# Kernel optimization log

Measured on AMD Instinct MI355X. Metric: run time of the kernel, lower is better.

Reference implementation:

```python
import jax, jax.numpy as jnp
import numpy as np

D_MODEL = 1024
N_HEADS = 16
HEAD_DIM = D_MODEL // N_HEADS
WINDOW = 512


def _rope(q, k, seq_len, head_dim):
    # interleaved RoPE, identical to the torch implementation
    theta = 1.0 / 10000.0 ** (jnp.arange(0, head_dim, 2, dtype=jnp.float32) / head_dim)
    pos = jnp.arange(seq_len, dtype=jnp.float32)
    freqs = jnp.outer(pos, theta)                      # [S, hD/2]
    cos_f = jnp.cos(freqs)[None, None]                 # [1,1,S,hD/2]
    sin_f = jnp.sin(freqs)[None, None]

    def rotate(x):
        x1, x2 = x[..., ::2], x[..., 1::2]
        return jnp.stack([x1 * cos_f - x2 * sin_f, x1 * sin_f + x2 * cos_f], axis=-1).reshape(x.shape)

    return rotate(q), rotate(k)


def _sliding_window_attn(q, k, v, W, scale):
    # chunked O(S*W) causal sliding-window attention
    B, nH, S, hD = q.shape
    n_chunks = (S + W - 1) // W
    pad_s = n_chunks * W - S
    k_pad = jnp.pad(k, ((0, 0), (0, 0), (W, pad_s), (0, 0)))
    v_pad = jnp.pad(v, ((0, 0), (0, 0), (W, pad_s), (0, 0)))
    q_pad = jnp.pad(q, ((0, 0), (0, 0), (0, pad_s), (0, 0)))
    q_c = q_pad.reshape(B, nH, n_chunks, W, hD)
    k_r = k_pad.reshape(B, nH, n_chunks + 1, W, hD)
    v_r = v_pad.reshape(B, nH, n_chunks + 1, W, hD)
    # window i = chunks [i, i+1] of the left-padded sequence (== torch unfold)
    k_c = jnp.concatenate([k_r[:, :, :-1], k_r[:, :, 1:]], axis=3)  # [B,nH,C,2W,hD]
    v_c = jnp.concatenate([v_r[:, :, :-1], v_r[:, :, 1:]], axis=3)
    attn = jnp.einsum('bhcqd,bhckd->bhcqk', q_c, k_c) * scale

    qi = jnp.arange(W)[:, None]
    ki = jnp.arange(2 * W)[None, :]
    cw_mask = (ki <= qi) | (ki > qi + W)               # [W, 2W]
    chunk_idx = jnp.arange(n_chunks)[:, None]
    abs_k = chunk_idx * W + ki - W                     # [C, 2W]
    pad_mask = (abs_k < 0) | (abs_k >= S)
    q_pos = jnp.arange(n_chunks * W).reshape(n_chunks, W)
    full_mask = cw_mask[None] | pad_mask[:, None, :] | (q_pos >= S)[..., None]  # [C,W,2W]

    attn = jnp.where(full_mask[None, None], -jnp.inf, attn)
    attn = jax.nn.softmax(attn, axis=-1)
    attn = jnp.nan_to_num(attn, nan=0.0)
    out = jnp.einsum('bhcqk,bhckd->bhcqd', attn, v_c)
    return out.reshape(B, nH, n_chunks * W, hD)[:, :, :S]


def _rmsnorm(x, w):
    eps = jnp.finfo(x.dtype).eps
    return x * jax.lax.rsqrt(jnp.mean(x * x, axis=-1, keepdims=True) + eps) * w


def _sdpa(q, k, v, scale):
    s = jnp.einsum('bhqd,bhkd->bhqk', q, k) * scale
    return jnp.einsum('bhqk,bhkd->bhqd', jax.nn.softmax(s, axis=-1), v)


def setup_inputs() -> dict:
    key = jax.random.key(0)
    ks = jax.random.split(key, 11)
    D = D_MODEL
    std = 0.02
    return {
        'x': jax.random.normal(ks[0], (2, 4096, D), jnp.float32),
        'landmarks': jax.random.normal(ks[1], (2, 256, D), jnp.float32),
        'archived_landmarks': jax.random.normal(ks[2], (2, 128, D), jnp.float32),
        'W_qkv': jax.random.normal(ks[3], (D, 3 * D), jnp.float32) * std,
        'W_lm': jax.random.normal(ks[4], (D, 2 * D), jnp.float32) * std,
        'W_arch': jax.random.normal(ks[5], (D, 2 * D), jnp.float32) * std,
        'W_o': jax.random.normal(ks[6], (D, D), jnp.float32) * std,
        'W_gate': jax.random.normal(ks[7], (3 * D, 2 * D), jnp.float32) * std,
        'g_local': jnp.ones((D,), jnp.float32),
        'g_lm': jnp.ones((D,), jnp.float32),
        'g_arch': jnp.ones((D,), jnp.float32),
    }


def reference(x, landmarks, archived_landmarks, W_qkv, W_lm, W_arch, W_o, W_gate, g_local, g_lm, g_arch):
    B, S, D = x.shape
    nH, hD = N_HEADS, HEAD_DIM
    scale = hD ** -0.5

    def rsh(t, L):
        return jnp.transpose(t.reshape(B, L, nH, hD), (0, 2, 1, 3))

    q, k, v = jnp.split(x @ W_qkv, 3, axis=-1)
    Q, K, V = rsh(q, S), rsh(k, S), rsh(v, S)
    Q, K = _rope(Q, K, S, hD)

    Weff = min(WINDOW, S)
    out_loc = _sliding_window_attn(Q, K, V, Weff, scale)  # S > Weff -> chunked path
    out_loc = _rmsnorm(jnp.transpose(out_loc, (0, 2, 1, 3)).reshape(B, S, D), g_local)

    L = landmarks.shape[1]
    K_lm, V_lm = jnp.split(landmarks @ W_lm, 2, axis=-1)
    out_lm = _sdpa(Q, rsh(K_lm, L), rsh(V_lm, L), scale)
    out_lm = _rmsnorm(jnp.transpose(out_lm, (0, 2, 1, 3)).reshape(B, S, D), g_lm)

    A = archived_landmarks.shape[1]
    K_a, V_a = jnp.split(archived_landmarks @ W_arch, 2, axis=-1)
    out_a = _sdpa(Q, rsh(K_a, A), rsh(V_a, A), scale)
    out_a = _rmsnorm(jnp.transpose(out_a, (0, 2, 1, 3)).reshape(B, S, D), g_arch)

    concat = jnp.concatenate([out_loc, out_lm, out_a], axis=-1)
    gate, value = jnp.split(concat @ W_gate, 2, axis=-1)
    return (jax.nn.silu(gate) * value) @ W_o
```

## Files before the change

### kernel.cpp

```cpp
#include <hip/hip_runtime.h>
#include <cstdint>
#include <cstddef>

typedef __bf16 bf16;
typedef __bf16 bf16x2 __attribute__((ext_vector_type(2)));
typedef __bf16 bf16x4 __attribute__((ext_vector_type(4)));
typedef __bf16 bf16x8 __attribute__((ext_vector_type(8)));
typedef float  f32x2 __attribute__((ext_vector_type(2)));
typedef float  f32x4 __attribute__((ext_vector_type(4)));

#define DEVFN __device__ __forceinline__
#define BAR()  asm volatile("s_barrier" ::: "memory")
#define VMW0() asm volatile("s_waitcnt vmcnt(0)" ::: "memory")
#define VMW3() asm volatile("s_waitcnt vmcnt(3)" ::: "memory")
#define VMW4() asm volatile("s_waitcnt vmcnt(4)" ::: "memory")

DEVFN void gld_lds16(void* lds, const void* g) {
  __builtin_amdgcn_global_load_lds(
      (__attribute__((address_space(1))) void*)g,
      (__attribute__((address_space(3))) void*)lds,
      16, 0, 0);
}

__global__ void cast_f32_bf16(const float* __restrict__ in, bf16* __restrict__ out, int n4) {
  int i = blockIdx.x * blockDim.x + threadIdx.x;
  if (i < n4) {
    f32x4 v = reinterpret_cast<const f32x4*>(in)[i];
    bf16x4 o;
    o[0] = (bf16)v[0]; o[1] = (bf16)v[1]; o[2] = (bf16)v[2]; o[3] = (bf16)v[3];
    reinterpret_cast<bf16x4*>(out)[i] = o;
  }
}

__global__ void transpose_cast(const float* __restrict__ in, bf16* __restrict__ out,
                               int R, int C) {
  __shared__ float t[32][33];
  int tx = threadIdx.x, ty = threadIdx.y;
  int c = blockIdx.x * 32 + tx;
  #pragma unroll
  for (int j = 0; j < 4; ++j) {
    int r = blockIdx.y * 32 + ty + j * 8;
    t[ty + j * 8][tx] = in[(size_t)r * C + c];
  }
  __syncthreads();
  int rr = blockIdx.y * 32 + tx;
  #pragma unroll
  for (int j = 0; j < 4; ++j) {
    int cc = blockIdx.x * 32 + ty + j * 8;
    out[(size_t)cc * R + rr] = (bf16)t[tx][ty + j * 8];
  }
}

__global__ void rope_table(float* __restrict__ tab) {
  int idx = blockIdx.x * 256 + threadIdx.x;
  int s = idx >> 5, i = idx & 31;
  float theta = powf(10000.f, -(float)(2 * i) * (1.f / 64.f));
  float f = (float)s * theta;
  tab[idx * 2]     = cosf(f);
  tab[idx * 2 + 1] = sinf(f);
}

template<typename OT>
__global__ __launch_bounds__(512) void gemm256(
    const bf16* __restrict__ A, const bf16* __restrict__ Bt, OT* __restrict__ C,
    int M, int N, int K) {
  __shared__ alignas(16) bf16 lds[2][2][2][256 * 32];
  const int tid = threadIdx.x;
  const int w = tid >> 6, l = tid & 63;
  const int l15 = l & 15, lg = l >> 4;
  const int wm = w >> 2, wn = w & 3;
  const int nwg = gridDim.x, qx = nwg >> 3;
  const int swz = (blockIdx.x & 7) * qx + (blockIdx.x >> 3);
  const int gx = N >> 8;
  const int m0 = (swz / gx) << 8;
  const int n0 = (swz % gx) << 8;
  const int nt = K >> 6;

  auto stage = [&](int b, int ab, int kk, int t) {
    const bf16* __restrict__ src = ab ? Bt : A;
    const int base0 = ab ? n0 : m0;
    const int k0 = (t << 6) + (kk << 5);
    #pragma unroll
    for (int i = 0; i < 2; ++i) {
      int u = i * 512 + tid;
      int row = u >> 2, slot = u & 3;
      int sslot = slot ^ ((row >> 1) & 3);
      gld_lds16(&lds[b][ab][kk][(i * 512 + w * 64) * 8],
                src + (size_t)(base0 + row) * K + k0 + sslot * 8);
    }
  };
  auto rd = [&](int b, int ab, int kk, int r) -> bf16x8 {
    return *reinterpret_cast<const bf16x8*>(
        &lds[b][ab][kk][(r << 5) + ((lg ^ ((r >> 1) & 3)) << 3)]);
  };

  f32x4 acc[8][4] = {};
  bf16x8 aLo[4], aHi[4], bfr[4];

  stage(0, 0, 0, 0);
  stage(0, 1, 0, 0);
  stage(0, 0, 1, 0);
  stage(0, 1, 1, 0);
  VMW4();
  BAR();

  for (int t = 0; t < nt; ++t) {
    const int c = t & 1;
    const bool st = (t + 1) < nt;
    #pragma unroll
    for (int f = 0; f < 4; ++f) aLo[f] = rd(c, 0, 0, wm * 128 + f * 16 + l15);
    #pragma unroll
    for (int f = 0; f < 4; ++f) bfr[f] = rd(c, 1, 0, wn * 64 + f * 16 + l15);
    if (st) stage(c ^ 1, 0, 0, t + 1);
    BAR();
    __builtin_amdgcn_s_setprio(1);
    #pragma unroll
    for (int mi = 0; mi < 4; ++mi)
      #pragma unroll
      for (int ni = 0; ni < 4; ++ni)
        acc[mi][ni] = __builtin_amdgcn_mfma_f32_16x16x32_bf16(aLo[mi], bfr[ni], acc[mi][ni], 0, 0, 0);
    __builtin_amdgcn_s_setprio(0);
    #pragma unroll
    for (int f = 0; f < 4; ++f) aHi[f] = rd(c, 0, 0, wm * 128 + (f + 4) * 16 + l15);
    BAR();
    if (st) stage(c ^ 1, 1, 0, t + 1);
    BAR();
    __builtin_amdgcn_s_setprio(1);
    #pragma unroll
    for (int mi = 0; mi < 4; ++mi)
      #pragma unroll
      for (int ni = 0; ni < 4; ++ni)
        acc[mi + 4][ni] = __builtin_amdgcn_mfma_f32_16x16x32_bf16(aHi[mi], bfr[ni], acc[mi + 4][ni], 0, 0, 0);
    __builtin_amdgcn_s_setprio(0);
    if (st) { VMW4(); } else { VMW0(); }
    BAR();
    #pragma unroll
    for (int f = 0; f < 4; ++f) aLo[f] = rd(c, 0, 1, wm * 128 + f * 16 + l15);
    #pragma unroll
    for (int f = 0; f < 4; ++f) bfr[f] = rd(c, 1, 1, wn * 64 + f * 16 + l15);
    if (st) stage(c ^ 1, 0, 1, t + 1);
    BAR();
    __builtin_amdgcn_s_setprio(1);
    #pragma unroll
    for (int mi = 0; mi < 4; ++mi)
      #pragma unroll
      for (int ni = 0; ni < 4; ++ni)
        acc[mi][ni] = __builtin_amdgcn_mfma_f32_16x16x32_bf16(aLo[mi], bfr[ni], acc[mi][ni], 0, 0, 0);
    __builtin_amdgcn_s_setprio(0);
    #pragma unroll
    for (int f = 0; f < 4; ++f) aHi[f] = rd(c, 0, 1, wm * 128 + (f + 4) * 16 + l15);
    BAR();
    if (st) stage(c ^ 1, 1, 1, t + 1);
    BAR();
    __builtin_amdgcn_s_setprio(1);
    #pragma unroll
    for (int mi = 0; mi < 4; ++mi)
      #pragma unroll
      for (int ni = 0; ni < 4; ++ni)
        acc[mi + 4][ni] = __builtin_amdgcn_mfma_f32_16x16x32_bf16(aHi[mi], bfr[ni], acc[mi + 4][ni], 0, 0, 0);
    __builtin_amdgcn_s_setprio(0);
    VMW4();
    BAR();
  }

  #pragma unroll
  for (int mi = 0; mi < 8; ++mi) {
    #pragma unroll
    for (int r = 0; r < 4; ++r) {
      int row = m0 + wm * 128 + mi * 16 + lg * 4 + r;
      OT* crow = C + (size_t)row * N + n0 + wn * 64 + l15;
      #pragma unroll
      for (int ni = 0; ni < 4; ++ni) crow[ni * 16] = (OT)acc[mi][ni][r];
    }
  }
}

template<typename OT>
__global__ __launch_bounds__(512) void gemm256n128(
    const bf16* __restrict__ A, const bf16* __restrict__ Bt, OT* __restrict__ C,
    int M, int N, int K) {
  __shared__ alignas(16) bf16 ldsA[2][2][256 * 32];
  __shared__ alignas(16) bf16 ldsB[2][2][128 * 32];
  const int tid = threadIdx.x;
  const int w = tid >> 6, l = tid & 63;
  const int l15 = l & 15, lg = l >> 4;
  const int wm = w >> 1, wn = w & 1;
  const int nwg = gridDim.x, qx = nwg >> 3;
  const int swz = (blockIdx.x & 7) * qx + (blockIdx.x >> 3);
  const int gx = N >> 7;
  const int m0 = (swz / gx) << 8;
  const int n0 = (swz % gx) << 7;
  const int nt = K >> 6;

  auto stageA = [&](int b, int kk, int t) {
    const int k0 = (t << 6) + (kk << 5);
    #pragma unroll
    for (int i = 0; i < 2; ++i) {
      int u = i * 512 + tid;
      int row = u >> 2, slot = u & 3;
      int ss = slot ^ ((row >> 1) & 3);
      gld_lds16(&ldsA[b][kk][(i * 512 + w * 64) * 8],
                A + (size_t)(m0 + row) * K + k0 + ss * 8);
    }
  };
  auto stageB = [&](int b, int kk, int t) {
    const int k0 = (t << 6) + (kk << 5);
    int row = tid >> 2, slot = tid & 3;
    int ss = slot ^ ((row >> 1) & 3);
    gld_lds16(&ldsB[b][kk][(w * 64) * 8],
              Bt + (size_t)(n0 + row) * K + k0 + ss * 8);
  };
  auto rdA = [&](int b, int kk, int r) -> bf16x8 {
    return *reinterpret_cast<const bf16x8*>(
        &ldsA[b][kk][(r << 5) + ((lg ^ ((r >> 1) & 3)) << 3)]);
  };
  auto rdB = [&](int b, int kk, int r) -> bf16x8 {
    return *reinterpret_cast<const bf16x8*>(
        &ldsB[b][kk][(r << 5) + ((lg ^ ((r >> 1) & 3)) << 3)]);
  };

  f32x4 acc[4][4] = {};
  bf16x8 af[4], bf[4];

  stageA(0, 0, 0); stageB(0, 0, 0);
  stageA(0, 1, 0); stageB(0, 1, 0);
  VMW3();
  BAR();

  for (int t = 0; t < nt; ++t) {
    const int c = t & 1;
    const bool st = (t + 1) < nt;
    #pragma unroll
    for (int kk = 0; kk < 2; ++kk) {
      #pragma unroll
      for (int f = 0; f < 4; ++f) af[f] = rdA(c, kk, wm * 64 + f * 16 + l15);
      #pragma unroll
      for (int f = 0; f < 4; ++f) bf[f] = rdB(c, kk, wn * 64 + f * 16 + l15);
      if (st) { stageA(c ^ 1, kk, t + 1); stageB(c ^ 1, kk, t + 1); }
      BAR();
      __builtin_amdgcn_s_setprio(1);
      #pragma unroll
      for (int mi = 0; mi < 4; ++mi)
        #pragma unroll
        for (int ni = 0; ni < 4; ++ni)
          acc[mi][ni] = __builtin_amdgcn_mfma_f32_16x16x32_bf16(af[mi], bf[ni], acc[mi][ni], 0, 0, 0);
      __builtin_amdgcn_s_setprio(0);
      if (st) { VMW3(); } else if (kk == 0) { VMW0(); }
      BAR();
    }
  }

  #pragma unroll
  for (int mi = 0; mi < 4; ++mi) {
    #pragma unroll
    for (int r = 0; r < 4; ++r) {
      int row = m0 + wm * 64 + mi * 16 + lg * 4 + r;
      OT* crow = C + (size_t)row * N + n0 + wn * 64 + l15;
      #pragma unroll
      for (int ni = 0; ni < 4; ++ni) crow[ni * 16] = (OT)acc[mi][ni][r];
    }
  }
}

template<typename OT>
__global__ __launch_bounds__(256) void gemm_bf16(
    const bf16* __restrict__ A, const bf16* __restrict__ Bt, OT* __restrict__ C,
    int M, int N, int K) {
  __shared__ alignas(16) bf16 As[128 * 64];
  __shared__ alignas(16) bf16 Bs[128 * 64];
  int tid = threadIdx.x;
  int w = tid >> 6, l = tid & 63;
  int l15 = l & 15, lg = l >> 4;
  int m0 = blockIdx.y * 128;
  int n0 = blockIdx.x * 128;
  int wr = (w >> 1) * 64, wc = (w & 1) * 64;
  f32x4 acc[4][4] = {};
  const size_t aBase = (size_t)m0 * K;
  const size_t bBase = (size_t)n0 * K;
  int nk = K >> 6;
  for (int kt = 0; kt < nk; ++kt) {
    int k0 = kt << 6;
    #pragma unroll
    for (int it = 0; it < 4; ++it) {
      int c = it * 256 + tid;
      int row = c >> 3, c8 = c & 7;
      gld_lds16(&As[(size_t)(it * 256 + w * 64) * 8],
                A + aBase + (size_t)row * K + k0 + c8 * 8);
      gld_lds16(&Bs[(size_t)(it * 256 + w * 64) * 8],
                Bt + bBase + (size_t)row * K + k0 + c8 * 8);
    }
    __syncthreads();
    #pragma unroll
    for (int kk = 0; kk < 64; kk += 32) {
      bf16x8 a[4], b[4];
      #pragma unroll
      for (int i = 0; i < 4; ++i)
        a[i] = *reinterpret_cast<const bf16x8*>(&As[(wr + i * 16 + l15) * 64 + kk + lg * 8]);
      #pragma unroll
      for (int i = 0; i < 4; ++i)
        b[i] = *reinterpret_cast<const bf16x8*>(&Bs[(wc + i * 16 + l15) * 64 + kk + lg * 8]);
      #pragma unroll
      for (int mi = 0; mi < 4; ++mi)
        #pragma unroll
        for (int ni = 0; ni < 4; ++ni)
          acc[mi][ni] = __builtin_amdgcn_mfma_f32_16x16x32_bf16(a[mi], b[ni], acc[mi][ni], 0, 0, 0);
    }
    __syncthreads();
  }
  #pragma unroll
  for (int mi = 0; mi < 4; ++mi) {
    #pragma unroll
    for (int r = 0; r < 4; ++r) {
      int row = m0 + wr + mi * 16 + lg * 4 + r;
      OT* crow = C + (size_t)row * N + n0 + wc + l15;
      #pragma unroll
      for (int ni = 0; ni < 4; ++ni) crow[ni * 16] = (OT)acc[mi][ni][r];
    }
  }
}

__global__ void rope_qk(const bf16* __restrict__ qkv, const float* __restrict__ tab,
                        bf16* __restrict__ Qb, bf16* __restrict__ Kb) {
  int idx = blockIdx.x * 256 + threadIdx.x;
  int i = idx & 31;
  int h = (idx >> 5) & 15;
  int bs = idx >> 9;
  int s = bs & 4095;
  int b = bs >> 12;
  const bf16* row = qkv + (size_t)bs * 3072;
  bf16x2 q2 = *reinterpret_cast<const bf16x2*>(row + h * 64 + 2 * i);
  bf16x2 k2 = *reinterpret_cast<const bf16x2*>(row + 1024 + h * 64 + 2 * i);
  f32x2 cs = *reinterpret_cast<const f32x2*>(tab + s * 64 + 2 * i);
  float c = cs[0], sn = cs[1];
  float q0 = (float)q2[0], q1 = (float)q2[1];
  float k0 = (float)k2[0], k1 = (float)k2[1];
  size_t ob = (((size_t)(b * 16 + h) * 4096) + s) * 64 + 2 * i;
  bf16x2 qo, ko;
  qo[0] = (bf16)((q0 * c - q1 * sn) * 0.125f);
  qo[1] = (bf16)((q0 * sn + q1 * c) * 0.125f);
  ko[0] = (bf16)(k0 * c - k1 * sn);
  ko[1] = (bf16)(k0 * sn + k1 * c);
  *reinterpret_cast<bf16x2*>(Qb + ob) = qo;
  *reinterpret_cast<bf16x2*>(Kb + ob) = ko;
}

__global__ void kv_post(const bf16* __restrict__ kv, bf16* __restrict__ Kdst,
                        bf16* __restrict__ Vt, int Lk, int rs, int koff, int voff) {
  __shared__ float t[64][65];
  int s0 = blockIdx.x * 64;
  int h = blockIdx.y, b = blockIdx.z;
  int tid = threadIdx.x;
  int lane_d = tid & 63;
  int rq = tid >> 6;
  const bf16* base = kv + (size_t)b * Lk * rs;
  if (Kdst) {
    #pragma unroll
    for (int r = 0; r < 16; ++r) {
      int si = r * 4 + rq;
      Kdst[(((size_t)(b * 16 + h) * Lk) + s0 + si) * 64 + lane_d] =
          base[(size_t)(s0 + si) * rs + koff + h * 64 + lane_d];
    }
  }
  #pragma unroll
  for (int r = 0; r < 16; ++r) {
    int si = r * 4 + rq;
    t[si][lane_d] = (float)base[(size_t)(s0 + si) * rs + voff + h * 64 + lane_d];
  }
  __syncthreads();
  #pragma unroll
  for (int r = 0; r < 16; ++r) {
    int d = r * 4 + rq;
    Vt[(((size_t)(b * 16 + h) * 64) + d) * Lk + s0 + lane_d] = (bf16)t[lane_d][d];
  }
}

template<bool WINDOWED>
__global__ __launch_bounds__(256) void attn_kernel(
    const bf16* __restrict__ Qb, const bf16* __restrict__ Kb, const bf16* __restrict__ Vt,
    bf16* __restrict__ outc, int S, int Lk, int col_off) {
  __shared__ alignas(16) bf16 Ks[64 * 64];
  __shared__ alignas(16) bf16 Vs[64 * 64];
  __shared__ alignas(16) bf16 Ps[4][16 * 72];
  int tid = threadIdx.x;
  int w = tid >> 6, l = tid & 63;
  int l15 = l & 15, lg = l >> 4;
  int qt = blockIdx.x, h = blockIdx.y, b = blockIdx.z;

  size_t qrow = (((size_t)(b * 16 + h) * S) + qt * 64 + w * 16 + l15) * 64;
  bf16x8 qf[2];
  qf[0] = *reinterpret_cast<const bf16x8*>(Qb + qrow + lg * 8);
  qf[1] = *reinterpret_cast<const bf16x8*>(Qb + qrow + 32 + lg * 8);
  const bf16* Kbase = Kb + ((size_t)(b * 16 + h) * Lk) * 64;
  const bf16* Vbase = Vt + ((size_t)(b * 16 + h) * 64) * Lk;

  float mrow = -1e30f, lsum = 0.f;
  f32x4 acc[4] = {};

  int kt_hi, kt_lo;
  if (WINDOWED) { kt_hi = qt; kt_lo = qt >= 8 ? qt - 8 : 0; }
  else          { kt_hi = (Lk >> 6) - 1; kt_lo = 0; }

  for (int kt = kt_hi; kt >= kt_lo; --kt) {
    const bf16* kg = Kbase + (size_t)kt * 64 * 64;
    #pragma unroll
    for (int it = 0; it < 2; ++it) {
      int u = it * 256 + tid;
      int row = u >> 3, sl = u & 7;
      gld_lds16(&Ks[(it * 256 + w * 64) * 8], kg + row * 64 + (sl ^ (row & 7)) * 8);
    }
    #pragma unroll
    for (int it = 0; it < 2; ++it) {
      int u = it * 256 + tid;
      int row = u >> 3, sl = u & 7;
      gld_lds16(&Vs[(it * 256 + w * 64) * 8],
                Vbase + (size_t)row * Lk + kt * 64 + (sl ^ (row & 7)) * 8);
    }
    __syncthreads();

    f32x4 st[4] = {};
    #pragma unroll
    for (int kk = 0; kk < 2; ++kk) {
      #pragma unroll
      for (int f = 0; f < 4; ++f) {
        bf16x8 kf = *reinterpret_cast<const bf16x8*>(
            &Ks[(f * 16 + l15) * 64 + (((kk * 4 + lg) ^ (l15 & 7)) << 3)]);
        st[f] = __builtin_amdgcn_mfma_f32_16x16x32_bf16(kf, qf[kk], st[f], 0, 0, 0);
      }
    }

    if (WINDOWED) {
      int qi = w * 16 + l15;
      if (kt == qt) {
        #pragma unroll
        for (int f = 0; f < 4; ++f)
          #pragma unroll
          for (int r = 0; r < 4; ++r)
            if (f * 16 + lg * 4 + r > qi) st[f][r] = -1e30f;
      } else if (kt == qt - 8) {
        #pragma unroll
        for (int f = 0; f < 4; ++f)
          #pragma unroll
          for (int r = 0; r < 4; ++r)
            if (f * 16 + lg * 4 + r <= qi) st[f][r] = -1e30f;
      }
    }

    float rm = -1e30f;
    #pragma unroll
    for (int f = 0; f < 4; ++f)
      #pragma unroll
      for (int r = 0; r < 4; ++r) rm = fmaxf(rm, st[f][r]);
    rm = fmaxf(rm, __shfl_xor(rm, 16));
    rm = fmaxf(rm, __shfl_xor(rm, 32));
    float mnew = fmaxf(mrow, rm);
    float fsc = __expf(mrow - mnew);
    float ps = 0.f;
    bf16x4 pv[4];
    #pragma unroll
    for (int f = 0; f < 4; ++f)
      #pragma unroll
      for (int r = 0; r < 4; ++r) {
        float p = __expf(st[f][r] - mnew);
        ps += p;
        pv[f][r] = (bf16)p;
      }
    ps += __shfl_xor(ps, 16);
    ps += __shfl_xor(ps, 32);
    lsum = lsum * fsc + ps;
    mrow = mnew;

    #pragma unroll
    for (int f = 0; f < 4; ++f)
      *reinterpret_cast<bf16x4*>(&Ps[w][l15 * 72 + f * 16 + lg * 4]) = pv[f];

    #pragma unroll
    for (int r = 0; r < 4; ++r) {
      float fr = __shfl(fsc, lg * 4 + r);
      #pragma unroll
      for (int f = 0; f < 4; ++f) acc[f][r] *= fr;
    }

    #pragma unroll
    for (int kk = 0; kk < 2; ++kk) {
      bf16x8 pa = *reinterpret_cast<const bf16x8*>(&Ps[w][l15 * 72 + kk * 32 + lg * 8]);
      #pragma unroll
      for (int f = 0; f < 4; ++f) {
        bf16x8 vf = *reinterpret_cast<const bf16x8*>(
            &Vs[(f * 16 + l15) * 64 + (((kk * 4 + lg) ^ (l15 & 7)) << 3)]);
        acc[f] = __builtin_amdgcn_mfma_f32_16x16x32_bf16(pa, vf, acc[f], 0, 0, 0);
      }
    }
    __syncthreads();
  }

  float inv = 1.f / lsum;
  #pragma unroll
  for (int r = 0; r < 4; ++r) {
    float ir = __shfl(inv, lg * 4 + r);
    int srow = qt * 64 + w * 16 + lg * 4 + r;
    bf16* orow = outc + ((size_t)b * S + srow) * 3072 + col_off + h * 64 + l15;
    #pragma unroll
    for (int f = 0; f < 4; ++f) orow[f * 16] = (bf16)(acc[f][r] * ir);
  }
}

__global__ __launch_bounds__(256) void rmsnorm_kernel(
    bf16* data, const float* __restrict__ g0,
    const float* __restrict__ g1, const float* __restrict__ g2) {
  int token = blockIdx.x;
  int seg = blockIdx.y;
  const float* g = seg == 0 ? g0 : (seg == 1 ? g1 : g2);
  int tid = threadIdx.x;
  size_t base = (size_t)token * 3072 + seg * 1024;
  bf16x4 bv = reinterpret_cast<const bf16x4*>(data + base)[tid];
  f32x4 v;
  #pragma unroll
  for (int j = 0; j < 4; ++j) v[j] = (float)bv[j];
  float ss = v[0] * v[0] + v[1] * v[1] + v[2] * v[2] + v[3] * v[3];
  #pragma unroll
  for (int m = 1; m < 64; m <<= 1) ss += __shfl_xor(ss, m);
  __shared__ float red[4];
  if ((tid & 63) == 0) red[tid >> 6] = ss;
  __syncthreads();
  float tot = red[0] + red[1] + red[2] + red[3];
  float sc = rsqrtf(tot * (1.f / 1024.f) + 1.19209290e-07f);
  f32x4 gv = reinterpret_cast<const f32x4*>(g)[tid];
  bf16x4 o;
  #pragma unroll
  for (int j = 0; j < 4; ++j) o[j] = (bf16)(v[j] * sc * gv[j]);
  reinterpret_cast<bf16x4*>(data + base)[tid] = o;
}

__global__ void silu_kernel(const bf16* __restrict__ gv, bf16* __restrict__ out) {
  int T = blockIdx.x * 256 + threadIdx.x;
  int row = T >> 8, c4 = (T & 255) * 4;
  bf16x4 g = *reinterpret_cast<const bf16x4*>(gv + (size_t)row * 2048 + c4);
  bf16x4 vv = *reinterpret_cast<const bf16x4*>(gv + (size_t)row * 2048 + 1024 + c4);
  bf16x4 o;
  #pragma unroll
  for (int j = 0; j < 4; ++j) {
    float x = (float)g[j];
    o[j] = (bf16)((x / (1.f + __expf(-x))) * (float)vv[j]);
  }
  *reinterpret_cast<bf16x4*>(out + (size_t)row * 1024 + c4) = o;
}

extern "C" void kernel_launch(void* const* d_in, const int* in_sizes, int n_in,
                              void* d_out, int out_size, void* d_ws, size_t ws_size,
                              hipStream_t stream) {
  (void)in_sizes; (void)n_in; (void)out_size; (void)ws_size;
  const float* x       = (const float*)d_in[0];
  const float* lm      = (const float*)d_in[1];
  const float* arch    = (const float*)d_in[2];
  const float* W_qkv   = (const float*)d_in[3];
  const float* W_lm    = (const float*)d_in[4];
  const float* W_arch  = (const float*)d_in[5];
  const float* W_o     = (const float*)d_in[6];
  const float* W_gate  = (const float*)d_in[7];
  const float* g_local = (const float*)d_in[8];
  const float* g_lm    = (const float*)d_in[9];
  const float* g_arch  = (const float*)d_in[10];
  float* out = (float*)d_out;

  char* ws = (char*)d_ws;
  size_t off = 0;
  auto alloc = [&](size_t bytes) -> void* {
    void* p = ws + off;
    off += (bytes + 255) & ~(size_t)255;
    return p;
  };
  bf16*  Wqkv_t   = (bf16*) alloc(3072ull * 1024 * 2);
  bf16*  Wlm_t    = (bf16*) alloc(2048ull * 1024 * 2);
  bf16*  Warch_t  = (bf16*) alloc(2048ull * 1024 * 2);
  bf16*  Wgate_t  = (bf16*) alloc(2048ull * 3072 * 2);
  bf16*  Wo_t     = (bf16*) alloc(1024ull * 1024 * 2);
  bf16*  lm_bf    = (bf16*) alloc(512ull * 1024 * 2);
  bf16*  arch_bf  = (bf16*) alloc(256ull * 1024 * 2);
  float* ropetab  = (float*)alloc(4096ull * 64 * 4);
  bf16*  Klm      = (bf16*) alloc(2ull * 16 * 256 * 64 * 2);
  bf16*  Vlm_t    = (bf16*) alloc(2ull * 16 * 64 * 256 * 2);
  bf16*  Ka       = (bf16*) alloc(2ull * 16 * 128 * 64 * 2);
  bf16*  Va_t     = (bf16*) alloc(2ull * 16 * 64 * 128 * 2);
  bf16*  lmkv_bf  = (bf16*) alloc(512ull * 2048 * 2);
  bf16*  akv_bf   = (bf16*) alloc(256ull * 2048 * 2);
  char* R1 = (char*)alloc(8192ull * 1024 * 2);
  bf16* x_bf  = (bf16*)R1;
  bf16* gated = (bf16*)R1;
  char* R2 = (char*)alloc(8192ull * 3072 * 2);
  bf16* qkv_bf  = (bf16*)R2;
  bf16* concatb = (bf16*)R2;
  char* R3 = (char*)alloc(3ull * 16 * 1024 * 1024);
  bf16* Qb = (bf16*)R3;
  bf16* Kb = (bf16*)(R3 + 16ull * 1024 * 1024);
  bf16* Vt = (bf16*)(R3 + 32ull * 1024 * 1024);
  bf16* gv = (bf16*)R3;

  transpose_cast<<<dim3(96, 32), dim3(32, 8), 0, stream>>>(W_qkv, Wqkv_t, 1024, 3072);
  transpose_cast<<<dim3(64, 32), dim3(32, 8), 0, stream>>>(W_lm, Wlm_t, 1024, 2048);
  transpose_cast<<<dim3(64, 32), dim3(32, 8), 0, stream>>>(W_arch, Warch_t, 1024, 2048);
  transpose_cast<<<dim3(64, 96), dim3(32, 8), 0, stream>>>(W_gate, Wgate_t, 3072, 2048);
  transpose_cast<<<dim3(32, 32), dim3(32, 8), 0, stream>>>(W_o, Wo_t, 1024, 1024);
  cast_f32_bf16<<<8192, 256, 0, stream>>>(x, x_bf, 8192 * 1024 / 4);
  cast_f32_bf16<<<512, 256, 0, stream>>>(lm, lm_bf, 512 * 1024 / 4);
  cast_f32_bf16<<<256, 256, 0, stream>>>(arch, arch_bf, 256 * 1024 / 4);
  rope_table<<<512, 256, 0, stream>>>(ropetab);

  gemm256n128<bf16><<<32 * 24, 512, 0, stream>>>(x_bf, Wqkv_t, qkv_bf, 8192, 3072, 1024);
  gemm_bf16<bf16><<<dim3(16, 4), 256, 0, stream>>>(lm_bf, Wlm_t, lmkv_bf, 512, 2048, 1024);
  gemm_bf16<bf16><<<dim3(16, 2), 256, 0, stream>>>(arch_bf, Warch_t, akv_bf, 256, 2048, 1024);

  rope_qk<<<16384, 256, 0, stream>>>(qkv_bf, ropetab, Qb, Kb);
  kv_post<<<dim3(64, 16, 2), 256, 0, stream>>>(qkv_bf, nullptr, Vt, 4096, 3072, 0, 2048);
  kv_post<<<dim3(4, 16, 2), 256, 0, stream>>>(lmkv_bf, Klm, Vlm_t, 256, 2048, 0, 1024);
  kv_post<<<dim3(2, 16, 2), 256, 0, stream>>>(akv_bf, Ka, Va_t, 128, 2048, 0, 1024);

  attn_kernel<true><<<dim3(64, 16, 2), 256, 0, stream>>>(Qb, Kb, Vt, concatb, 4096, 4096, 0);
  attn_kernel<false><<<dim3(64, 16, 2), 256, 0, stream>>>(Qb, Klm, Vlm_t, concatb, 4096, 256, 1024);
  attn_kernel<false><<<dim3(64, 16, 2), 256, 0, stream>>>(Qb, Ka, Va_t, concatb, 4096, 128, 2048);

  rmsnorm_kernel<<<dim3(8192, 3), 256, 0, stream>>>(concatb, g_local, g_lm, g_arch);

  gemm256<bf16><<<32 * 8, 512, 0, stream>>>(concatb, Wgate_t, gv, 8192, 2048, 3072);
  silu_kernel<<<8192, 256, 0, stream>>>(gv, gated);
  gemm256n128<float><<<32 * 8, 512, 0, stream>>>(gated, Wo_t, out, 8192, 1024, 1024);
}
```

Baseline: 417.6 us.

## Restructure attention kernels: double-buffered windowed attention and resident-KV landmark attention

Replaces the generic attention kernel with two specialized kernels. The windowed kernel processes 128 queries per block (two 16-row groups per wave), reusing each loaded K/V tile across twice as many queries, and double-buffers K/V tiles so the next tile loads while the current one is computed. The landmark/archive kernel loads the whole small K/V set into LDS once per block and loops over 512 queries with 8 waves, removing repeated tile loads and barriers. This costs more registers and LDS per block, which may lower occupancy, and the windowed grid shrinks to half the blocks.

```diff
diff --git a/kernel.cpp b/kernel.cpp
--- a/kernel.cpp
+++ b/kernel.cpp
@@ -14,6 +14,7 @@
 #define VMW0() asm volatile("s_waitcnt vmcnt(0)" ::: "memory")
 #define VMW3() asm volatile("s_waitcnt vmcnt(3)" ::: "memory")
 #define VMW4() asm volatile("s_waitcnt vmcnt(4)" ::: "memory")
+#define MFMA16 __builtin_amdgcn_mfma_f32_16x16x32_bf16
 
 DEVFN void gld_lds16(void* lds, const void* g) {
   __builtin_amdgcn_global_load_lds(
@@ -118,7 +119,7 @@
     for (int mi = 0; mi < 4; ++mi)
       #pragma unroll
       for (int ni = 0; ni < 4; ++ni)
-        acc[mi][ni] = __builtin_amdgcn_mfma_f32_16x16x32_bf16(aLo[mi], bfr[ni], acc[mi][ni], 0, 0, 0);
+        acc[mi][ni] = MFMA16(aLo[mi], bfr[ni], acc[mi][ni], 0, 0, 0);
     __builtin_amdgcn_s_setprio(0);
     #pragma unroll
     for (int f = 0; f < 4; ++f) aHi[f] = rd(c, 0, 0, wm * 128 + (f + 4) * 16 + l15);
@@ -130,7 +131,7 @@
     for (int mi = 0; mi < 4; ++mi)
       #pragma unroll
       for (int ni = 0; ni < 4; ++ni)
-        acc[mi + 4][ni] = __builtin_amdgcn_mfma_f32_16x16x32_bf16(aHi[mi], bfr[ni], acc[mi + 4][ni], 0, 0, 0);
+        acc[mi + 4][ni] = MFMA16(aHi[mi], bfr[ni], acc[mi + 4][ni], 0, 0, 0);
     __builtin_amdgcn_s_setprio(0);
     if (st) { VMW4(); } else { VMW0(); }
     BAR();
@@ -145,7 +146,7 @@
     for (int mi = 0; mi < 4; ++mi)
       #pragma unroll
       for (int ni = 0; ni < 4; ++ni)
-        acc[mi][ni] = __builtin_amdgcn_mfma_f32_16x16x32_bf16(aLo[mi], bfr[ni], acc[mi][ni], 0, 0, 0);
+        acc[mi][ni] = MFMA16(aLo[mi], bfr[ni], acc[mi][ni], 0, 0, 0);
     __builtin_amdgcn_s_setprio(0);
     #pragma unroll
     for (int f = 0; f < 4; ++f) aHi[f] = rd(c, 0, 1, wm * 128 + (f + 4) * 16 + l15);
@@ -157,7 +158,7 @@
     for (int mi = 0; mi < 4; ++mi)
       #pragma unroll
       for (int ni = 0; ni < 4; ++ni)
-        acc[mi + 4][ni] = __builtin_amdgcn_mfma_f32_16x16x32_bf16(aHi[mi], bfr[ni], acc[mi + 4][ni], 0, 0, 0);
+        acc[mi + 4][ni] = MFMA16(aHi[mi], bfr[ni], acc[mi + 4][ni], 0, 0, 0);
     __builtin_amdgcn_s_setprio(0);
     VMW4();
     BAR();
@@ -243,9 +244,10 @@
       for (int mi = 0; mi < 4; ++mi)
         #pragma unroll
         for (int ni = 0; ni < 4; ++ni)
-          acc[mi][ni] = __builtin_amdgcn_mfma_f32_16x16x32_bf16(af[mi], bf[ni], acc[mi][ni], 0, 0, 0);
+          acc[mi][ni] = MFMA16(af[mi], bf[ni], acc[mi][ni], 0, 0, 0);
       __builtin_amdgcn_s_setprio(0);
-      if (st) { VMW3(); } else if (kk == 0) { VMW0(); }
+      if (st) { VMW3(); }
+      else if (kk == 0) { VMW0(); }
       BAR();
     }
   }
@@ -303,7 +305,7 @@
       for (int mi = 0; mi < 4; ++mi)
         #pragma unroll
         for (int ni = 0; ni < 4; ++ni)
-          acc[mi][ni] = __builtin_amdgcn_mfma_f32_16x16x32_bf16(a[mi], b[ni], acc[mi][ni], 0, 0, 0);
+          acc[mi][ni] = MFMA16(a[mi], b[ni], acc[mi][ni], 0, 0, 0);
     }
     __syncthreads();
   }
@@ -374,133 +376,286 @@
   }
 }
 
-template<bool WINDOWED>
-__global__ __launch_bounds__(256) void attn_kernel(
-    const bf16* __restrict__ Qb, const bf16* __restrict__ Kb, const bf16* __restrict__ Vt,
-    bf16* __restrict__ outc, int S, int Lk, int col_off) {
-  __shared__ alignas(16) bf16 Ks[64 * 64];
-  __shared__ alignas(16) bf16 Vs[64 * 64];
-  __shared__ alignas(16) bf16 Ps[4][16 * 72];
-  int tid = threadIdx.x;
-  int w = tid >> 6, l = tid & 63;
-  int l15 = l & 15, lg = l >> 4;
-  int qt = blockIdx.x, h = blockIdx.y, b = blockIdx.z;
-
-  size_t qrow = (((size_t)(b * 16 + h) * S) + qt * 64 + w * 16 + l15) * 64;
-  bf16x8 qf[2];
-  qf[0] = *reinterpret_cast<const bf16x8*>(Qb + qrow + lg * 8);
-  qf[1] = *reinterpret_cast<const bf16x8*>(Qb + qrow + 32 + lg * 8);
-  const bf16* Kbase = Kb + ((size_t)(b * 16 + h) * Lk) * 64;
-  const bf16* Vbase = Vt + ((size_t)(b * 16 + h) * 64) * Lk;
-
-  float mrow = -1e30f, lsum = 0.f;
-  f32x4 acc[4] = {};
-
-  int kt_hi, kt_lo;
-  if (WINDOWED) { kt_hi = qt; kt_lo = qt >= 8 ? qt - 8 : 0; }
-  else          { kt_hi = (Lk >> 6) - 1; kt_lo = 0; }
-
-  for (int kt = kt_hi; kt >= kt_lo; --kt) {
+__global__ __launch_bounds__(256) void attn_win(
+    const bf16* __restrict__ Qb, const bf16* __restrict__ Kb,
+    const bf16* __restrict__ Vt, bf16* __restrict__ outc) {
+  constexpr int S = 4096;
+  __shared__ alignas(16) bf16 Ks[2][64 * 64];
+  __shared__ alignas(16) bf16 Vs[2][64 * 64];
+  __shared__ alignas(16) bf16 Ps[4][2][16 * 72];
+  const int tid = threadIdx.x;
+  const int w = tid >> 6, l = tid & 63;
+  const int l15 = l & 15, lg = l >> 4;
+  const int h = blockIdx.y, b = blockIdx.z;
+  const int Q0 = blockIdx.x * 128;
+  const int qt0 = Q0 >> 6;
+
+  const bf16* Kbase = Kb + ((size_t)(b * 16 + h) * S) * 64;
+  const bf16* Vbase = Vt + ((size_t)(b * 16 + h) * 64) * S;
+
+  bf16x8 qf[2][2];
+  #pragma unroll
+  for (int c = 0; c < 2; ++c) {
+    size_t qrow = (((size_t)(b * 16 + h) * S) + Q0 + w * 32 + c * 16 + l15) * 64;
+    qf[c][0] = *reinterpret_cast<const bf16x8*>(Qb + qrow + lg * 8);
+    qf[c][1] = *reinterpret_cast<const bf16x8*>(Qb + qrow + 32 + lg * 8);
+  }
+
+  const int kt_hi = qt0 + 1;
+  const int kt_lo = qt0 >= 8 ? qt0 - 8 : 0;
+
+  auto stage = [&](int buf, int kt) {
     const bf16* kg = Kbase + (size_t)kt * 64 * 64;
     #pragma unroll
     for (int it = 0; it < 2; ++it) {
       int u = it * 256 + tid;
       int row = u >> 3, sl = u & 7;
-      gld_lds16(&Ks[(it * 256 + w * 64) * 8], kg + row * 64 + (sl ^ (row & 7)) * 8);
+      gld_lds16(&Ks[buf][(it * 256 + w * 64) * 8], kg + row * 64 + (sl ^ (row & 7)) * 8);
     }
     #pragma unroll
     for (int it = 0; it < 2; ++it) {
       int u = it * 256 + tid;
       int row = u >> 3, sl = u & 7;
-      gld_lds16(&Vs[(it * 256 + w * 64) * 8],
-                Vbase + (size_t)row * Lk + kt * 64 + (sl ^ (row & 7)) * 8);
-    }
-    __syncthreads();
-
-    f32x4 st[4] = {};
+      gld_lds16(&Vs[buf][(it * 256 + w * 64) * 8],
+                Vbase + (size_t)row * S + kt * 64 + (sl ^ (row & 7)) * 8);
+    }
+  };
+
+  float mrow[2] = {-30000.f, -30000.f}, lsum[2] = {0.f, 0.f};
+  f32x4 acc[2][4] = {};
+
+  stage(0, kt_hi);
+
+  int i = 0;
+  for (int kt = kt_hi; kt >= kt_lo; --kt, ++i) {
+    const int buf = i & 1;
+    if (kt > kt_lo) { stage(buf ^ 1, kt - 1); VMW4(); } else { VMW0(); }
+    BAR();
+
+    f32x4 st[2][4] = {};
     #pragma unroll
     for (int kk = 0; kk < 2; ++kk) {
       #pragma unroll
       for (int f = 0; f < 4; ++f) {
         bf16x8 kf = *reinterpret_cast<const bf16x8*>(
-            &Ks[(f * 16 + l15) * 64 + (((kk * 4 + lg) ^ (l15 & 7)) << 3)]);
-        st[f] = __builtin_amdgcn_mfma_f32_16x16x32_bf16(kf, qf[kk], st[f], 0, 0, 0);
-      }
-    }
-
-    if (WINDOWED) {
-      int qi = w * 16 + l15;
-      if (kt == qt) {
+            &Ks[buf][(f * 16 + l15) * 64 + (((kk * 4 + lg) ^ (l15 & 7)) << 3)]);
+        #pragma unroll
+        for (int c = 0; c < 2; ++c)
+          st[c][f] = MFMA16(kf, qf[c][kk], st[c][f], 0, 0, 0);
+      }
+    }
+
+    if (kt >= qt0) {
+      #pragma unroll
+      for (int c = 0; c < 2; ++c) {
+        int q = Q0 + w * 32 + c * 16 + l15;
         #pragma unroll
         for (int f = 0; f < 4; ++f)
           #pragma unroll
           for (int r = 0; r < 4; ++r)
-            if (f * 16 + lg * 4 + r > qi) st[f][r] = -1e30f;
-      } else if (kt == qt - 8) {
+            if (kt * 64 + f * 16 + lg * 4 + r > q) st[c][f][r] = -1e30f;
+      }
+    }
+    if (kt <= qt0 - 7) {
+      #pragma unroll
+      for (int c = 0; c < 2; ++c) {
+        int q = Q0 + w * 32 + c * 16 + l15;
         #pragma unroll
         for (int f = 0; f < 4; ++f)
           #pragma unroll
           for (int r = 0; r < 4; ++r)
-            if (f * 16 + lg * 4 + r <= qi) st[f][r] = -1e30f;
-      }
-    }
-
-    float rm = -1e30f;
-    #pragma unroll
-    for (int f = 0; f < 4; ++f)
-      #pragma unroll
-      for (int r = 0; r < 4; ++r) rm = fmaxf(rm, st[f][r]);
-    rm = fmaxf(rm, __shfl_xor(rm, 16));
-    rm = fmaxf(rm, __shfl_xor(rm, 32));
-    float mnew = fmaxf(mrow, rm);
-    float fsc = __expf(mrow - mnew);
-    float ps = 0.f;
-    bf16x4 pv[4];
-    #pragma unroll
-    for (int f = 0; f < 4; ++f)
+            if (kt * 64 + f * 16 + lg * 4 + r <= q - 512) st[c][f][r] = -1e30f;
+      }
+    }
+
+    #pragma unroll
+    for (int c = 0; c < 2; ++c) {
+      float rm = -1e30f;
+      #pragma unroll
+      for (int f = 0; f < 4; ++f)
+        #pragma unroll
+        for (int r = 0; r < 4; ++r) rm = fmaxf(rm, st[c][f][r]);
+      rm = fmaxf(rm, __shfl_xor(rm, 16));
+      rm = fmaxf(rm, __shfl_xor(rm, 32));
+      float mnew = fmaxf(mrow[c], rm);
+      float fsc = __expf(mrow[c] - mnew);
+      float ps = 0.f;
+      #pragma unroll
+      for (int f = 0; f < 4; ++f) {
+        bf16x4 pv;
+        #pragma unroll
+        for (int r = 0; r < 4; ++r) {
+          float p = __expf(st[c][f][r] - mnew);
+          ps += p;
+          pv[r] = (bf16)p;
+        }
+        *reinterpret_cast<bf16x4*>(&Ps[w][c][l15 * 72 + f * 16 + lg * 4]) = pv;
+      }
+      ps += __shfl_xor(ps, 16);
+      ps += __shfl_xor(ps, 32);
+      lsum[c] = lsum[c] * fsc + ps;
+      mrow[c] = mnew;
       #pragma unroll
       for (int r = 0; r < 4; ++r) {
-        float p = __expf(st[f][r] - mnew);
-        ps += p;
-        pv[f][r] = (bf16)p;
-      }
-    ps += __shfl_xor(ps, 16);
-    ps += __shfl_xor(ps, 32);
-    lsum = lsum * fsc + ps;
-    mrow = mnew;
-
-    #pragma unroll
-    for (int f = 0; f < 4; ++f)
-      *reinterpret_cast<bf16x4*>(&Ps[w][l15 * 72 + f * 16 + lg * 4]) = pv[f];
-
-    #pragma unroll
-    for (int r = 0; r < 4; ++r) {
-      float fr = __shfl(fsc, lg * 4 + r);
-      #pragma unroll
-      for (int f = 0; f < 4; ++f) acc[f][r] *= fr;
+        float fr = __shfl(fsc, lg * 4 + r);
+        #pragma unroll
+        for (int f = 0; f < 4; ++f) acc[c][f][r] *= fr;
+      }
     }
 
     #pragma unroll
     for (int kk = 0; kk < 2; ++kk) {
-      bf16x8 pa = *reinterpret_cast<const bf16x8*>(&Ps[w][l15 * 72 + kk * 32 + lg * 8]);
+      bf16x8 pa[2];
+      #pragma unroll
+      for (int c = 0; c < 2; ++c)
+        pa[c] = *reinterpret_cast<const bf16x8*>(&Ps[w][c][l15 * 72 + kk * 32 + lg * 8]);
       #pragma unroll
       for (int f = 0; f < 4; ++f) {
         bf16x8 vf = *reinterpret_cast<const bf16x8*>(
-            &Vs[(f * 16 + l15) * 64 + (((kk * 4 + lg) ^ (l15 & 7)) << 3)]);
-        acc[f] = __builtin_amdgcn_mfma_f32_16x16x32_bf16(pa, vf, acc[f], 0, 0, 0);
-      }
-    }
-    __syncthreads();
-  }
-
-  float inv = 1.f / lsum;
-  #pragma unroll
-  for (int r = 0; r < 4; ++r) {
-    float ir = __shfl(inv, lg * 4 + r);
-    int srow = qt * 64 + w * 16 + lg * 4 + r;
-    bf16* orow = outc + ((size_t)b * S + srow) * 3072 + col_off + h * 64 + l15;
-    #pragma unroll
-    for (int f = 0; f < 4; ++f) orow[f * 16] = (bf16)(acc[f][r] * ir);
+            &Vs[buf][(f * 16 + l15) * 64 + (((kk * 4 + lg) ^ (l15 & 7)) << 3)]);
+        #pragma unroll
+        for (int c = 0; c < 2; ++c)
+          acc[c][f] = MFMA16(pa[c], vf, acc[c][f], 0, 0, 0);
+      }
+    }
+    BAR();
+  }
+
+  #pragma unroll
+  for (int c = 0; c < 2; ++c) {
+    float inv = 1.f / lsum[c];
+    #pragma unroll
+    for (int r = 0; r < 4; ++r) {
+      float ir = __shfl(inv, lg * 4 + r);
+      int srow = Q0 + w * 32 + c * 16 + lg * 4 + r;
+      bf16* orow = outc + ((size_t)b * S + srow) * 3072 + h * 64 + l15;
+      #pragma unroll
+      for (int f = 0; f < 4; ++f) orow[f * 16] = (bf16)(acc[c][f][r] * ir);
+    }
+  }
+}
+
+template<int LKV, int NQI>
+__global__ __launch_bounds__(512) void attn_res(
+    const bf16* __restrict__ Qb, const bf16* __restrict__ Kb,
+    const bf16* __restrict__ Vt, bf16* __restrict__ outc, int col_off) {
+  constexpr int S = 4096;
+  __shared__ alignas(16) bf16 Ks[LKV * 64];
+  __shared__ alignas(16) bf16 Vs[64 * LKV];
+  __shared__ alignas(16) bf16 Ps[8][2][16 * 72];
+  const int tid = threadIdx.x;
+  const int w = tid >> 6, l = tid & 63;
+  const int l15 = l & 15, lg = l >> 4;
+  const int h = blockIdx.y, b = blockIdx.z;
+  const bf16* Kg = Kb + ((size_t)(b * 16 + h) * LKV) * 64;
+  const bf16* Vg = Vt + ((size_t)(b * 16 + h) * 64) * LKV;
+
+  constexpr int NU = LKV / 64;
+  constexpr int SPR = LKV / 8;
+  #pragma unroll
+  for (int i = 0; i < NU; ++i) {
+    int u = i * 512 + tid;
+    int row = u >> 3, sl = u & 7;
+    gld_lds16(&Ks[(i * 512 + w * 64) * 8], Kg + row * 64 + (sl ^ (row & 7)) * 8);
+  }
+  #pragma unroll
+  for (int i = 0; i < NU; ++i) {
+    int u = i * 512 + tid;
+    int row = u / SPR, sl = u % SPR;
+    gld_lds16(&Vs[(i * 512 + w * 64) * 8],
+              Vg + (size_t)row * LKV + ((sl & ~7) + ((sl & 7) ^ (row & 7))) * 8);
+  }
+  __syncthreads();
+
+  for (int qi = 0; qi < NQI; ++qi) {
+    const int Q0 = (blockIdx.x * NQI + qi) * 256 + w * 32;
+    bf16x8 qf[2][2];
+    #pragma unroll
+    for (int c = 0; c < 2; ++c) {
+      size_t qrow = (((size_t)(b * 16 + h) * S) + Q0 + c * 16 + l15) * 64;
+      qf[c][0] = *reinterpret_cast<const bf16x8*>(Qb + qrow + lg * 8);
+      qf[c][1] = *reinterpret_cast<const bf16x8*>(Qb + qrow + 32 + lg * 8);
+    }
+    float mrow[2] = {-30000.f, -30000.f}, lsum[2] = {0.f, 0.f};
+    f32x4 acc[2][4] = {};
+
+    #pragma unroll
+    for (int kt = 0; kt < LKV / 64; ++kt) {
+      f32x4 st[2][4] = {};
+      #pragma unroll
+      for (int kk = 0; kk < 2; ++kk) {
+        #pragma unroll
+        for (int f = 0; f < 4; ++f) {
+          bf16x8 kf = *reinterpret_cast<const bf16x8*>(
+              &Ks[(kt * 64 + f * 16 + l15) * 64 + (((kk * 4 + lg) ^ (l15 & 7)) << 3)]);
+          #pragma unroll
+          for (int c = 0; c < 2; ++c)
+            st[c][f] = MFMA16(kf, qf[c][kk], st[c][f], 0, 0, 0);
+        }
+      }
+      #pragma unroll
+      for (int c = 0; c < 2; ++c) {
+        float rm = -1e30f;
+        #pragma unroll
+        for (int f = 0; f < 4; ++f)
+          #pragma unroll
+          for (int r = 0; r < 4; ++r) rm = fmaxf(rm, st[c][f][r]);
+        rm = fmaxf(rm, __shfl_xor(rm, 16));
+        rm = fmaxf(rm, __shfl_xor(rm, 32));
+        float mnew = fmaxf(mrow[c], rm);
+        float fsc = __expf(mrow[c] - mnew);
+        float ps = 0.f;
+        #pragma unroll
+        for (int f = 0; f < 4; ++f) {
+          bf16x4 pv;
+          #pragma unroll
+          for (int r = 0; r < 4; ++r) {
+            float p = __expf(st[c][f][r] - mnew);
+            ps += p;
+            pv[r] = (bf16)p;
+          }
+          *reinterpret_cast<bf16x4*>(&Ps[w][c][l15 * 72 + f * 16 + lg * 4]) = pv;
+        }
+        ps += __shfl_xor(ps, 16);
+        ps += __shfl_xor(ps, 32);
+        lsum[c] = lsum[c] * fsc + ps;
+        mrow[c] = mnew;
+        #pragma unroll
+        for (int r = 0; r < 4; ++r) {
+          float fr = __shfl(fsc, lg * 4 + r);
+          #pragma unroll
+          for (int f = 0; f < 4; ++f) acc[c][f][r] *= fr;
+        }
+      }
+      #pragma unroll
+      for (int kk = 0; kk < 2; ++kk) {
+        bf16x8 pa[2];
+        #pragma unroll
+        for (int c = 0; c < 2; ++c)
+          pa[c] = *reinterpret_cast<const bf16x8*>(&Ps[w][c][l15 * 72 + kk * 32 + lg * 8]);
+        #pragma unroll
+        for (int f = 0; f < 4; ++f) {
+          bf16x8 vf = *reinterpret_cast<const bf16x8*>(
+              &Vs[(f * 16 + l15) * LKV + ((kt * 8 + ((kk * 4 + lg) ^ (l15 & 7))) << 3)]);
+          #pragma unroll
+          for (int c = 0; c < 2; ++c)
+            acc[c][f] = MFMA16(pa[c], vf, acc[c][f], 0, 0, 0);
+        }
+      }
+    }
+
+    #pragma unroll
+    for (int c = 0; c < 2; ++c) {
+      float inv = 1.f / lsum[c];
+      #pragma unroll
+      for (int r = 0; r < 4; ++r) {
+        float ir = __shfl(inv, lg * 4 + r);
+        int srow = Q0 + c * 16 + lg * 4 + r;
+        bf16* orow = outc + ((size_t)b * S + srow) * 3072 + col_off + h * 64 + l15;
+        #pragma unroll
+        for (int f = 0; f < 4; ++f) orow[f * 16] = (bf16)(acc[c][f][r] * ir);
+      }
+    }
   }
 }
 
@@ -614,9 +769,9 @@
   kv_post<<<dim3(4, 16, 2), 256, 0, stream>>>(lmkv_bf, Klm, Vlm_t, 256, 2048, 0, 1024);
   kv_post<<<dim3(2, 16, 2), 256, 0, stream>>>(akv_bf, Ka, Va_t, 128, 2048, 0, 1024);
 
-  attn_kernel<true><<<dim3(64, 16, 2), 256, 0, stream>>>(Qb, Kb, Vt, concatb, 4096, 4096, 0);
-  attn_kernel<false><<<dim3(64, 16, 2), 256, 0, stream>>>(Qb, Klm, Vlm_t, concatb, 4096, 256, 1024);
-  attn_kernel<false><<<dim3(64, 16, 2), 256, 0, stream>>>(Qb, Ka, Va_t, concatb, 4096, 128, 2048);
+  attn_win<<<dim3(32, 16, 2), 256, 0, stream>>>(Qb, Kb, Vt, concatb);
+  attn_res<256, 2><<<dim3(8, 16, 2), 512, 0, stream>>>(Qb, Klm, Vlm_t, concatb, 1024);
+  attn_res<128, 2><<<dim3(8, 16, 2), 512, 0, stream>>>(Qb, Ka, Va_t, concatb, 2048);
 
   rmsnorm_kernel<<<dim3(8192, 3), 256, 0, stream>>>(concatb, g_local, g_lm, g_arch);
 
```

Result: slower. 448.0 us (+7.3%).
